# Kernel optimization log

Hardware: AMD Instinct MI355X
Metric: run time of the kernel (lower is better)

The kernel has to match this reference:

```python
import jax, jax.numpy as jnp
import numpy as np

NEG = -1.0e9

def setup_inputs() -> dict:
    key = jax.random.key(0)
    ks = jax.random.split(key, 8)
    B, H, S, D = 4, 8, 1024, 64
    Q = jax.random.normal(ks[0], (B, H, S, D), dtype=jnp.float32)
    K = jax.random.normal(ks[1], (B, H, S, D), dtype=jnp.float32)
    V = jax.random.normal(ks[2], (B, H, S, D), dtype=jnp.float32)
    attn_mask_col = jax.random.randint(ks[3], (B, H, S, S), 0, 2).astype(jnp.bool_)
    adj_matrix = jax.random.uniform(ks[4], (B, H, S, S), dtype=jnp.float32)
    dist_matrix = jax.random.uniform(ks[5], (B, H, S, S), dtype=jnp.float32)
    conv_w = jax.random.normal(ks[6], (3,), dtype=jnp.float32)
    conv_b = jax.random.normal(ks[7], (1,), dtype=jnp.float32)
    return {"Q": Q, "K": K, "V": V, "attn_mask_col": attn_mask_col,
            "adj_matrix": adj_matrix, "dist_matrix": dist_matrix,
            "conv_w": conv_w, "conv_b": conv_b}

def reference(Q, K, V, attn_mask_col, adj_matrix, dist_matrix, conv_w, conv_b):
    d_k = Q.shape[-1]
    # scores: [B,H,Sq,Sk]
    scores = jnp.einsum('bhqd,bhkd->bhqk', Q, K) / jnp.sqrt(jnp.float32(d_k))
    scores = jnp.where(attn_mask_col, NEG, scores)
    scores = jax.nn.softmax(scores, axis=-1)
    # 1x1 Conv2d(3->1) over stacked [scores, dist, adj] == learned weighted sum
    weighted = conv_w[0] * scores + conv_w[1] * dist_matrix + conv_w[2] * adj_matrix + conv_b[0]
    weighted = jnp.where(attn_mask_col, NEG, weighted)
    attn = jax.nn.softmax(weighted, axis=-1)  # dropout p=0 -> identity
    context = jnp.einsum('bhqk,bhkd->bhqd', attn, V)
    return (context, attn)
```

## Files before the change

### kernel.cpp

```cpp
#include <hip/hip_runtime.h>

typedef _Float16 f16;
typedef _Float16 f16x8 __attribute__((ext_vector_type(8)));
typedef _Float16 f16x4 __attribute__((ext_vector_type(4)));
typedef float f32x4 __attribute__((ext_vector_type(4)));
typedef int   i32x4 __attribute__((ext_vector_type(4)));

constexpr int B_ = 4, H_ = 8, S_ = 1024, D_ = 64;
constexpr int BQ = 16;
constexpr int NT = 512;
constexpr int KC = 128;
constexpr int QH_LD = 72;
constexpr int SC_LD = 1032;
constexpr float LOG2E = 1.44269504f;

__device__ __forceinline__ float wred(float v) {
#pragma unroll
  for (int off = 32; off > 0; off >>= 1) v += __shfl_xor(v, off);
  return v;
}

__global__ __launch_bounds__(NT)
void fused_attn(const float* __restrict__ Q, const float* __restrict__ K,
                const float* __restrict__ V, const int* __restrict__ mask,
                const float* __restrict__ adj, const float* __restrict__ dist,
                const float* __restrict__ cw, const float* __restrict__ cb,
                float* __restrict__ outC, float* __restrict__ outA)
{
  __shared__ __align__(16) f16 Qh[BQ * QH_LD];
  __shared__ __align__(16) f16 sch[BQ * SC_LD];
  __shared__ float rs1w[8][16];
  __shared__ float rinv2[BQ];

  const int tid = threadIdx.x;
  const int sw = (blockIdx.x & 7) * 256 + (blockIdx.x >> 3);
  const int qt = sw & 63;
  const int bh = sw >> 6;
  const int q0 = qt * BQ;
  const int wv = tid >> 6;
  const int ln = tid & 63;
  const int lg = ln >> 4;
  const int li = ln & 15;

  const float* Qp = Q + ((size_t)bh * S_ + q0) * D_;
  const float* Kp = K + (size_t)bh * S_ * D_;
  const float* Vp = V + (size_t)bh * S_ * D_;
  const size_t rb = ((size_t)bh * S_ + q0) * S_;

  if (tid < 256) {
    const int q = tid >> 4, c4 = (tid & 15) << 2;
    float4 v = *(const float4*)(Qp + q * D_ + c4);
    f16* d = &Qh[q * QH_LD + c4];
    d[0] = (f16)v.x; d[1] = (f16)v.y; d[2] = (f16)v.z; d[3] = (f16)v.w;
  }
  const float w0 = cw[0], w1 = cw[1], w2 = cw[2], bb = cb[0];
  __syncthreads();

  f16x8 aq0 = *(const f16x8*)&Qh[li * QH_LD + 0 * 32 + lg * 8];
  f16x8 aq1 = *(const f16x8*)&Qh[li * QH_LD + 1 * 32 + lg * 8];

  const int n0 = wv * 16;
  float rs[4] = {0.f, 0.f, 0.f, 0.f};
#pragma unroll 2
  for (int c = 0; c < 8; ++c) {
    const int kg = c * KC + n0 + li;
    const float* Kr = Kp + (size_t)kg * D_ + lg * 8;
    const float4 ka = *(const float4*)(Kr + 0);
    const float4 kb = *(const float4*)(Kr + 4);
    const float4 kc2 = *(const float4*)(Kr + 32);
    const float4 kd = *(const float4*)(Kr + 36);
    f16x8 b0, b1;
    b0[0] = (f16)ka.x; b0[1] = (f16)ka.y; b0[2] = (f16)ka.z; b0[3] = (f16)ka.w;
    b0[4] = (f16)kb.x; b0[5] = (f16)kb.y; b0[6] = (f16)kb.z; b0[7] = (f16)kb.w;
    b1[0] = (f16)kc2.x; b1[1] = (f16)kc2.y; b1[2] = (f16)kc2.z; b1[3] = (f16)kc2.w;
    b1[4] = (f16)kd.x; b1[5] = (f16)kd.y; b1[6] = (f16)kd.z; b1[7] = (f16)kd.w;
    f32x4 acc = {0.f, 0.f, 0.f, 0.f};
    acc = __builtin_amdgcn_mfma_f32_16x16x32_f16(aq0, b0, acc, 0, 0, 0);
    acc = __builtin_amdgcn_mfma_f32_16x16x32_f16(aq1, b1, acc, 0, 0, 0);
#pragma unroll
    for (int r = 0; r < 4; ++r) {
      const int m = lg * 4 + r;
      const f16 ef = (f16)exp2f(acc[r] * (0.125f * LOG2E));
      sch[m * SC_LD + kg] = ef;
      rs[r] += (float)ef;
    }
  }
#pragma unroll
  for (int r = 0; r < 4; ++r) {
    rs[r] += __shfl_xor(rs[r], 1); rs[r] += __shfl_xor(rs[r], 2);
    rs[r] += __shfl_xor(rs[r], 4); rs[r] += __shfl_xor(rs[r], 8);
  }
  if (li == 0) {
#pragma unroll
    for (int r = 0; r < 4; ++r) rs1w[wv][lg * 4 + r] = rs[r];
  }
  __syncthreads();

#pragma unroll
  for (int rr = 0; rr < 2; ++rr) {
    const int q = 2 * wv + rr;
    const size_t base = rb + (size_t)q * S_;
    const int k0 = ln * 4;
    const i32x4 mv0 = __builtin_nontemporal_load((const i32x4*)(mask + base + k0 + 0));
    const i32x4 mv1 = __builtin_nontemporal_load((const i32x4*)(mask + base + k0 + 256));
    const i32x4 mv2 = __builtin_nontemporal_load((const i32x4*)(mask + base + k0 + 512));
    const i32x4 mv3 = __builtin_nontemporal_load((const i32x4*)(mask + base + k0 + 768));
    const f32x4 dv0 = __builtin_nontemporal_load((const f32x4*)(dist + base + k0 + 0));
    const f32x4 dv1 = __builtin_nontemporal_load((const f32x4*)(dist + base + k0 + 256));
    const f32x4 dv2 = __builtin_nontemporal_load((const f32x4*)(dist + base + k0 + 512));
    const f32x4 dv3 = __builtin_nontemporal_load((const f32x4*)(dist + base + k0 + 768));
    const f32x4 av0 = __builtin_nontemporal_load((const f32x4*)(adj + base + k0 + 0));
    const f32x4 av1 = __builtin_nontemporal_load((const f32x4*)(adj + base + k0 + 256));
    const f32x4 av2 = __builtin_nontemporal_load((const f32x4*)(adj + base + k0 + 512));
    const f32x4 av3 = __builtin_nontemporal_load((const f32x4*)(adj + base + k0 + 768));
    const f16x4 ef0 = *(const f16x4*)&sch[q * SC_LD + k0 + 0];
    const f16x4 ef1 = *(const f16x4*)&sch[q * SC_LD + k0 + 256];
    const f16x4 ef2 = *(const f16x4*)&sch[q * SC_LD + k0 + 512];
    const f16x4 ef3 = *(const f16x4*)&sch[q * SC_LD + k0 + 768];
    __builtin_amdgcn_sched_barrier(0);
    float corr =
        (mv0[0] ? (float)ef0[0] : 0.f) + (mv0[1] ? (float)ef0[1] : 0.f) +
        (mv0[2] ? (float)ef0[2] : 0.f) + (mv0[3] ? (float)ef0[3] : 0.f) +
        (mv1[0] ? (float)ef1[0] : 0.f) + (mv1[1] ? (float)ef1[1] : 0.f) +
        (mv1[2] ? (float)ef1[2] : 0.f) + (mv1[3] ? (float)ef1[3] : 0.f) +
        (mv2[0] ? (float)ef2[0] : 0.f) + (mv2[1] ? (float)ef2[1] : 0.f) +
        (mv2[2] ? (float)ef2[2] : 0.f) + (mv2[3] ? (float)ef2[3] : 0.f) +
        (mv3[0] ? (float)ef3[0] : 0.f) + (mv3[1] ? (float)ef3[1] : 0.f) +
        (mv3[2] ? (float)ef3[2] : 0.f) + (mv3[3] ? (float)ef3[3] : 0.f);
    float tq = 0.f;
#pragma unroll
    for (int w = 0; w < 8; ++w) tq += rs1w[w][q];
    corr = wred(corr);
    const float i1 = 1.f / (tq - corr);
    const float W0 = w0 * i1 * LOG2E, W1 = w1 * LOG2E, W2 = w2 * LOG2E;
    const float BBL = bb * LOG2E;
    f16x4 af0, af1, af2, af3;
    float s2 = 0.f;
#define CSM(AF, MV, DV, AV, EF)                                               \
    {                                                                         \
      const float t0 = fmaf(W0, (float)EF[0], fmaf(W1, DV[0], fmaf(W2, AV[0], BBL))); \
      const float t1 = fmaf(W0, (float)EF[1], fmaf(W1, DV[1], fmaf(W2, AV[1], BBL))); \
      const float t2 = fmaf(W0, (float)EF[2], fmaf(W1, DV[2], fmaf(W2, AV[2], BBL))); \
      const float t3 = fmaf(W0, (float)EF[3], fmaf(W1, DV[3], fmaf(W2, AV[3], BBL))); \
      const float a0 = MV[0] ? 0.f : exp2f(t0);                               \
      const float a1 = MV[1] ? 0.f : exp2f(t1);                               \
      const float a2 = MV[2] ? 0.f : exp2f(t2);                               \
      const float a3 = MV[3] ? 0.f : exp2f(t3);                               \
      AF[0] = (f16)a0; AF[1] = (f16)a1; AF[2] = (f16)a2; AF[3] = (f16)a3;     \
      s2 += a0 + a1 + a2 + a3;                                                \
    }
    CSM(af0, mv0, dv0, av0, ef0)
    CSM(af1, mv1, dv1, av1, ef1)
    CSM(af2, mv2, dv2, av2, ef2)
    CSM(af3, mv3, dv3, av3, ef3)
#undef CSM
    *(f16x4*)&sch[q * SC_LD + k0 + 0]   = af0;
    *(f16x4*)&sch[q * SC_LD + k0 + 256] = af1;
    *(f16x4*)&sch[q * SC_LD + k0 + 512] = af2;
    *(f16x4*)&sch[q * SC_LD + k0 + 768] = af3;
    s2 = wred(s2);
    const float i2 = 1.f / s2;
    if (ln == 0) rinv2[q] = i2;
    f32x4 o;
    o[0] = (float)af0[0] * i2; o[1] = (float)af0[1] * i2;
    o[2] = (float)af0[2] * i2; o[3] = (float)af0[3] * i2;
    __builtin_nontemporal_store(o, (f32x4*)(outA + base + k0 + 0));
    o[0] = (float)af1[0] * i2; o[1] = (float)af1[1] * i2;
    o[2] = (float)af1[2] * i2; o[3] = (float)af1[3] * i2;
    __builtin_nontemporal_store(o, (f32x4*)(outA + base + k0 + 256));
    o[0] = (float)af2[0] * i2; o[1] = (float)af2[1] * i2;
    o[2] = (float)af2[2] * i2; o[3] = (float)af2[3] * i2;
    __builtin_nontemporal_store(o, (f32x4*)(outA + base + k0 + 512));
    o[0] = (float)af3[0] * i2; o[1] = (float)af3[1] * i2;
    o[2] = (float)af3[2] * i2; o[3] = (float)af3[3] * i2;
    __builtin_nontemporal_store(o, (f32x4*)(outA + base + k0 + 768));
  }
  __syncthreads();

  const int ntile = wv >> 1;
  const int spair = (wv & 1) * 2;
  const int d0 = ntile * 16 + li;
  f32x4 cacc = {0.f, 0.f, 0.f, 0.f};
#pragma unroll 2
  for (int c = 0; c < 8; ++c) {
#pragma unroll
    for (int u = 0; u < 2; ++u) {
      const int s = spair + u;
      const float* Vc = Vp + (size_t)(c * KC + s * 32 + lg * 8) * D_ + d0;
      f16x8 bfr;
#pragma unroll
      for (int j = 0; j < 8; ++j) bfr[j] = (f16)Vc[(size_t)j * D_];
      f16x8 a = *(const f16x8*)&sch[li * SC_LD + c * KC + s * 32 + lg * 8];
      cacc = __builtin_amdgcn_mfma_f32_16x16x32_f16(a, bfr, cacc, 0, 0, 0);
    }
  }
  __syncthreads();
  float* fscr = reinterpret_cast<float*>(sch);
  *(f32x4*)&fscr[tid * 4] = cacc;
  __syncthreads();
  if (tid < 256) {
    const int t = tid >> 6, l2 = tid & 63;
    const int g2 = l2 >> 4, n = l2 & 15;
    f32x4 p  = *(const f32x4*)&fscr[((2 * t) * 64 + l2) * 4];
    f32x4 p2 = *(const f32x4*)&fscr[((2 * t + 1) * 64 + l2) * 4];
#pragma unroll
    for (int r = 0; r < 4; ++r) {
      const int m = g2 * 4 + r;
      outC[((size_t)bh * S_ + q0 + m) * D_ + t * 16 + n] = (p[r] + p2[r]) * rinv2[m];
    }
  }
}

extern "C" void kernel_launch(void* const* d_in, const int* in_sizes, int n_in,
                              void* d_out, int out_size, void* d_ws, size_t ws_size,
                              hipStream_t stream) {
  const float* Q    = (const float*)d_in[0];
  const float* K    = (const float*)d_in[1];
  const float* V    = (const float*)d_in[2];
  const int*   mask = (const int*)  d_in[3];
  const float* adj  = (const float*)d_in[4];
  const float* dist = (const float*)d_in[5];
  const float* cw   = (const float*)d_in[6];
  const float* cb   = (const float*)d_in[7];

  float* outC = (float*)d_out;
  float* outA = outC + (size_t)B_ * H_ * S_ * D_;

  fused_attn<<<dim3(B_ * H_ * (S_ / BQ)), NT, 0, stream>>>(
      Q, K, V, mask, adj, dist, cw, cb, outC, outA);
}
```

Before: 141.9 us.

## Halve block to 256 threads and drop cross-wave PV reduction

Shrinks each block from 8 to 4 wavefronts. Each wave now handles twice as many key chunks in the score phase, four query rows in the softmax phase, and a full 16-column output tile over all keys in the PV phase. This removes the shared-memory split-K reduction and its two barriers at the end. More blocks can be resident per CU, at the cost of less latency hiding and more serial work per wave inside each block.

```diff
diff --git a/kernel.cpp b/kernel.cpp
--- a/kernel.cpp
+++ b/kernel.cpp
@@ -8,8 +8,7 @@
 
 constexpr int B_ = 4, H_ = 8, S_ = 1024, D_ = 64;
 constexpr int BQ = 16;
-constexpr int NT = 512;
-constexpr int KC = 128;
+constexpr int NT = 256;
 constexpr int QH_LD = 72;
 constexpr int SC_LD = 1032;
 constexpr float LOG2E = 1.44269504f;
@@ -29,7 +28,7 @@
 {
   __shared__ __align__(16) f16 Qh[BQ * QH_LD];
   __shared__ __align__(16) f16 sch[BQ * SC_LD];
-  __shared__ float rs1w[8][16];
+  __shared__ float rs1w[4][16];
   __shared__ float rinv2[BQ];
 
   const int tid = threadIdx.x;
@@ -47,7 +46,7 @@
   const float* Vp = V + (size_t)bh * S_ * D_;
   const size_t rb = ((size_t)bh * S_ + q0) * S_;
 
-  if (tid < 256) {
+  {
     const int q = tid >> 4, c4 = (tid & 15) << 2;
     float4 v = *(const float4*)(Qp + q * D_ + c4);
     f16* d = &Qh[q * QH_LD + c4];
@@ -62,8 +61,8 @@
   const int n0 = wv * 16;
   float rs[4] = {0.f, 0.f, 0.f, 0.f};
 #pragma unroll 2
-  for (int c = 0; c < 8; ++c) {
-    const int kg = c * KC + n0 + li;
+  for (int c = 0; c < 16; ++c) {
+    const int kg = c * 64 + n0 + li;
     const float* Kr = Kp + (size_t)kg * D_ + lg * 8;
     const float4 ka = *(const float4*)(Kr + 0);
     const float4 kb = *(const float4*)(Kr + 4);
@@ -97,8 +96,8 @@
   __syncthreads();
 
 #pragma unroll
-  for (int rr = 0; rr < 2; ++rr) {
-    const int q = 2 * wv + rr;
+  for (int rr = 0; rr < 4; ++rr) {
+    const int q = 4 * wv + rr;
     const size_t base = rb + (size_t)q * S_;
     const int k0 = ln * 4;
     const i32x4 mv0 = __builtin_nontemporal_load((const i32x4*)(mask + base + k0 + 0));
@@ -129,7 +128,7 @@
         (mv3[2] ? (float)ef3[2] : 0.f) + (mv3[3] ? (float)ef3[3] : 0.f);
     float tq = 0.f;
 #pragma unroll
-    for (int w = 0; w < 8; ++w) tq += rs1w[w][q];
+    for (int w = 0; w < 4; ++w) tq += rs1w[w][q];
     corr = wred(corr);
     const float i1 = 1.f / (tq - corr);
     const float W0 = w0 * i1 * LOG2E, W1 = w1 * LOG2E, W2 = w2 * LOG2E;
@@ -177,37 +176,24 @@
   }
   __syncthreads();
 
-  const int ntile = wv >> 1;
-  const int spair = (wv & 1) * 2;
-  const int d0 = ntile * 16 + li;
+  const int d0 = wv * 16 + li;
   f32x4 cacc = {0.f, 0.f, 0.f, 0.f};
 #pragma unroll 2
   for (int c = 0; c < 8; ++c) {
 #pragma unroll
-    for (int u = 0; u < 2; ++u) {
-      const int s = spair + u;
-      const float* Vc = Vp + (size_t)(c * KC + s * 32 + lg * 8) * D_ + d0;
+    for (int s = 0; s < 4; ++s) {
+      const float* Vc = Vp + (size_t)(c * 128 + s * 32 + lg * 8) * D_ + d0;
       f16x8 bfr;
 #pragma unroll
       for (int j = 0; j < 8; ++j) bfr[j] = (f16)Vc[(size_t)j * D_];
-      f16x8 a = *(const f16x8*)&sch[li * SC_LD + c * KC + s * 32 + lg * 8];
+      f16x8 a = *(const f16x8*)&sch[li * SC_LD + c * 128 + s * 32 + lg * 8];
       cacc = __builtin_amdgcn_mfma_f32_16x16x32_f16(a, bfr, cacc, 0, 0, 0);
     }
   }
-  __syncthreads();
-  float* fscr = reinterpret_cast<float*>(sch);
-  *(f32x4*)&fscr[tid * 4] = cacc;
-  __syncthreads();
-  if (tid < 256) {
-    const int t = tid >> 6, l2 = tid & 63;
-    const int g2 = l2 >> 4, n = l2 & 15;
-    f32x4 p  = *(const f32x4*)&fscr[((2 * t) * 64 + l2) * 4];
-    f32x4 p2 = *(const f32x4*)&fscr[((2 * t + 1) * 64 + l2) * 4];
-#pragma unroll
-    for (int r = 0; r < 4; ++r) {
-      const int m = g2 * 4 + r;
-      outC[((size_t)bh * S_ + q0 + m) * D_ + t * 16 + n] = (p[r] + p2[r]) * rinv2[m];
-    }
+#pragma unroll
+  for (int r = 0; r < 4; ++r) {
+    const int m = lg * 4 + r;
+    outC[((size_t)bh * S_ + q0 + m) * D_ + d0] = cacc[r] * rinv2[m];
   }
 }
 
```

New measurement: 160.0 us. 1.13x slower.
